# Optimization experiments

Measured on AMD Instinct MI355X. Metric: run time of the kernel, lower is better.

Reference implementation:

```python
import jax, jax.numpy as jnp
import numpy as np

P = 8    # patch_size
N = 16   # n_patches
WS = 32  # window_size


def setup_inputs() -> dict:
    key = jax.random.key(0)
    k1, k2 = jax.random.split(key)
    B, C, H, W = 8, 12, 512, 512
    return {
        "data_real": jax.random.normal(k1, (B, C, H, W), dtype=jnp.float32),
        "data_imag": jax.random.normal(k2, (B, C, H, W), dtype=jnp.float32),
        "ref_x": 248,
        "ref_y": 248,
    }


def reference(data_real, data_imag, ref_x, ref_y):
    p, n, ws = P, N, WS
    # complex64 represented as trailing real/imag axis (matches torch.view_as_real)
    data = jnp.stack([data_real, data_imag], axis=-1)  # [B,C,H,W,2]
    B, C, H, W, _ = data.shape

    # reference patch at (ref_x, ref_y)
    ref = data[:, :, ref_x:ref_x + p, ref_y:ref_y + p, :]  # [B,C,p,p,2]

    # clamped search window (static Python ints -> static shapes)
    wx0 = max(ref_x - ws // 2, 0); wx1 = min(ref_x + ws // 2, H)
    wy0 = max(ref_y - ws // 2, 0); wy1 = min(ref_y + ws // 2, W)
    win = data[:, :, wx0:wx1, wy0:wy1, :]  # [B,C,Wh,Ww,2]
    Wh, Ww = win.shape[2], win.shape[3]
    Ph, Pw = Wh - p + 1, Ww - p + 1

    # all sliding patches in the window, vectorized via fancy indexing
    ix = jnp.arange(Ph)[:, None] + jnp.arange(p)[None, :]  # [Ph,p]
    iy = jnp.arange(Pw)[:, None] + jnp.arange(p)[None, :]  # [Pw,p]
    patches = win[:, :, ix[:, None, :, None], iy[None, :, None, :], :]  # [B,C,Ph,Pw,p,p,2]

    # mse_loss over view_as_real == 0.5 * mean(|diff|^2) over p*p complex elems
    diff = patches - ref[:, :, None, None]
    dists = 0.5 * jnp.mean(diff * diff, axis=(-3, -2, -1))  # [B,C,Ph,Pw]

    M = Ph * Pw  # row-major (x outer, y inner) matches the torch loop order
    dists = dists.reshape(B, C, M)
    pats = patches.reshape(B, C, M, p * p, 2)

    slot = jnp.arange(n)

    def select(dv, pv):  # dv: [M], pv: [M, p*p, 2]
        def step(carry, inp):
            nd, ns = carry
            di, pi = inp
            mask = nd > di                      # candidate slots
            oh = (slot == jnp.argmax(mask)) & jnp.any(mask)  # first True slot
            nd = jnp.where(oh, di, nd)
            ns = jnp.where(oh[:, None, None], pi, ns)
            return (nd, ns), None

        init = (jnp.full((n,), 1e33, dtype=dv.dtype),
                jnp.zeros((n, p * p, 2), dtype=pv.dtype))
        (nd, ns), _ = jax.lax.scan(step, init, (dv, pv))
        return ns

    # independent sequential top-n insertion per (batch, contrast)
    sims = jax.vmap(jax.vmap(select))(dists, pats)  # [B,C,n,p*p,2]
    return sims
```

## Files before the change

### kernel.cpp

```cpp
#include <hip/hip_runtime.h>
#include <math.h>

#define PP    8
#define NSEL  16
#define WSZ   32

__global__ __launch_bounds__(256) void patches_select_kernel(
    const float* __restrict__ d_re,
    const float* __restrict__ d_im,
    const int*   __restrict__ p_rx,
    const int*   __restrict__ p_ry,
    float*       __restrict__ out,
    int H, int W)
{
    const int bc  = blockIdx.x;
    const int tid = threadIdx.x;

    const int rx = p_rx[0];
    const int ry = p_ry[0];
    const int wx0 = max(rx - WSZ / 2, 0);
    const int wx1 = min(rx + WSZ / 2, H);
    const int wy0 = max(ry - WSZ / 2, 0);
    const int wy1 = min(ry + WSZ / 2, W);
    const int Wh = wx1 - wx0;
    const int Ww = wy1 - wy0;
    const int Ph = Wh - PP + 1;
    const int Pw = Ww - PP + 1;
    const int M  = Ph * Pw;
    const int Mpad = (M + 15) & ~15;

    __shared__ float sre[WSZ][WSZ];
    __shared__ float sim[WSZ][WSZ];
    __shared__ float sref[PP][PP][2];
    __shared__ float dists[WSZ * WSZ];
    __shared__ int   selIdx[NSEL];

    const size_t plane = (size_t)H * W;
    const float* baseR = d_re + (size_t)bc * plane;
    const float* baseI = d_im + (size_t)bc * plane;

    for (int t = tid; t < Wh * Ww; t += 256) {
        const int i = t / Ww, j = t - i * Ww;
        const size_t g = (size_t)(wx0 + i) * W + (wy0 + j);
        sre[i][j] = baseR[g];
        sim[i][j] = baseI[g];
    }
    for (int t = tid; t < PP * PP; t += 256) {
        const int i = t / PP, j = t - i * PP;
        const size_t g = (size_t)(rx + i) * W + (ry + j);
        sref[i][j][0] = baseR[g];
        sref[i][j][1] = baseI[g];
    }
    if (tid < 16 && M + tid < Mpad) dists[M + tid] = INFINITY;
    __syncthreads();

    for (int m = tid; m < M; m += 256) {
        const int pi = m / Pw, pj = m - pi * Pw;
        float r[8];
#pragma unroll
        for (int j = 0; j < 8; ++j) r[j] = 0.0f;
#pragma unroll
        for (int k = 0; k < 16; ++k) {
            const int dx  = k >> 1;
            const int dyb = (k & 1) * 4;
#pragma unroll
            for (int j = 0; j < 8; ++j) {
                const int dy   = dyb + (j >> 1);
                const int comp = j & 1;
                const float w  = comp ? sim[pi + dx][pj + dy] : sre[pi + dx][pj + dy];
                const float rf = sref[dx][dy][comp];
                const float dl = __fsub_rn(w, rf);
                const float sq = __fmul_rn(dl, dl);
                r[j] = __fadd_rn(r[j], sq);
            }
        }
        const float s0 = __fadd_rn(__fadd_rn(r[0], r[1]), __fadd_rn(r[2], r[3]));
        const float s1 = __fadd_rn(__fadd_rn(r[4], r[5]), __fadd_rn(r[6], r[7]));
        const float S  = __fadd_rn(s0, s1);
        dists[m] = S * (1.0f / 256.0f);
    }
    __syncthreads();

    if (tid < 64) {
        float nd  = (tid < NSEL) ? 1e33f : -1.0f;
        int   mi  = -1;
        float cur[16];
#pragma unroll
        for (int u = 0; u < 16; ++u) cur[u] = dists[u];
        for (int m0 = 0; m0 < Mpad; m0 += 16) {
            float nxt[16];
            const int nb = m0 + 16;
            if (nb < Mpad) {
#pragma unroll
                for (int u = 0; u < 16; ++u) nxt[u] = dists[nb + u];
            } else {
#pragma unroll
                for (int u = 0; u < 16; ++u) nxt[u] = INFINITY;
            }
#pragma unroll
            for (int u = 0; u < 16; ++u) {
                const unsigned long long mask = __ballot(nd > cur[u]);
                const int first = __ffsll(mask) - 1;
                if (tid == first) { nd = cur[u]; mi = m0 + u; }
            }
#pragma unroll
            for (int u = 0; u < 16; ++u) cur[u] = nxt[u];
        }
        if (tid < NSEL) selIdx[tid] = mi;
    }
    __syncthreads();

    float* obase = out + (size_t)bc * (NSEL * PP * PP * 2);
    for (int t = tid; t < NSEL * PP * PP * 2; t += 256) {
        const int slot = t >> 7;
        const int rem  = t & 127;
        const int k    = rem >> 1;
        const int comp = rem & 1;
        const int m    = selIdx[slot];
        float v = 0.0f;
        if (m >= 0) {
            const int pi = m / Pw, pj = m - pi * Pw;
            const int dx = k >> 3, dy = k & 7;
            v = comp ? sim[pi + dx][pj + dy] : sre[pi + dx][pj + dy];
        }
        obase[t] = v;
    }
}

extern "C" void kernel_launch(void* const* d_in, const int* in_sizes, int n_in,
                              void* d_out, int out_size, void* d_ws, size_t ws_size,
                              hipStream_t stream) {
    const float* d_re = (const float*)d_in[0];
    const float* d_im = (const float*)d_in[1];
    const int*   p_rx = (const int*)d_in[2];
    const int*   p_ry = (const int*)d_in[3];
    float* out = (float*)d_out;

    const int H = 512, W = 512;
    const int BC = in_sizes[0] / (H * W);

    patches_select_kernel<<<BC, 256, 0, stream>>>(d_re, d_im, p_rx, p_ry, out, H, W);
}
```

Measured before the change: 197.1 us.

## Interleave window in shared memory, skip non-inserting blocks in top-n scan

```diff
diff --git a/kernel.cpp b/kernel.cpp
--- a/kernel.cpp
+++ b/kernel.cpp
@@ -4,6 +4,14 @@
 #define PP    8
 #define NSEL  16
 #define WSZ   32
+
+__device__ __forceinline__ float min16(const float* a) {
+    const float m0 = fminf(fminf(a[0],  a[1]),  fminf(a[2],  a[3]));
+    const float m1 = fminf(fminf(a[4],  a[5]),  fminf(a[6],  a[7]));
+    const float m2 = fminf(fminf(a[8],  a[9]),  fminf(a[10], a[11]));
+    const float m3 = fminf(fminf(a[12], a[13]), fminf(a[14], a[15]));
+    return fminf(fminf(m0, m1), fminf(m2, m3));
+}
 
 __global__ __launch_bounds__(256) void patches_select_kernel(
     const float* __restrict__ d_re,
@@ -29,24 +37,32 @@
     const int M  = Ph * Pw;
     const int Mpad = (M + 15) & ~15;
 
-    __shared__ float sre[WSZ][WSZ];
-    __shared__ float sim[WSZ][WSZ];
+    __shared__ float swin[WSZ][WSZ][2];
     __shared__ float sref[PP][PP][2];
     __shared__ float dists[WSZ * WSZ];
-    __shared__ int   selIdx[NSEL];
+    __shared__ int   selPK[NSEL];
 
     const size_t plane = (size_t)H * W;
     const float* baseR = d_re + (size_t)bc * plane;
     const float* baseI = d_im + (size_t)bc * plane;
 
-    for (int t = tid; t < Wh * Ww; t += 256) {
-        const int i = t / Ww, j = t - i * Ww;
-        const size_t g = (size_t)(wx0 + i) * W + (wy0 + j);
-        sre[i][j] = baseR[g];
-        sim[i][j] = baseI[g];
+    if (Ww == WSZ) {
+        for (int t = tid; t < Wh * WSZ; t += 256) {
+            const int i = t >> 5, j = t & 31;
+            const size_t g = (size_t)(wx0 + i) * W + (wy0 + j);
+            swin[i][j][0] = baseR[g];
+            swin[i][j][1] = baseI[g];
+        }
+    } else {
+        for (int t = tid; t < Wh * Ww; t += 256) {
+            const int i = t / Ww, j = t - i * Ww;
+            const size_t g = (size_t)(wx0 + i) * W + (wy0 + j);
+            swin[i][j][0] = baseR[g];
+            swin[i][j][1] = baseI[g];
+        }
     }
     for (int t = tid; t < PP * PP; t += 256) {
-        const int i = t / PP, j = t - i * PP;
+        const int i = t >> 3, j = t & 7;
         const size_t g = (size_t)(rx + i) * W + (ry + j);
         sref[i][j][0] = baseR[g];
         sref[i][j][1] = baseI[g];
@@ -64,14 +80,14 @@
             const int dx  = k >> 1;
             const int dyb = (k & 1) * 4;
 #pragma unroll
-            for (int j = 0; j < 8; ++j) {
-                const int dy   = dyb + (j >> 1);
-                const int comp = j & 1;
-                const float w  = comp ? sim[pi + dx][pj + dy] : sre[pi + dx][pj + dy];
-                const float rf = sref[dx][dy][comp];
-                const float dl = __fsub_rn(w, rf);
-                const float sq = __fmul_rn(dl, dl);
-                r[j] = __fadd_rn(r[j], sq);
+            for (int dd = 0; dd < 4; ++dd) {
+                const int dy = dyb + dd;
+                const float2 wv = *reinterpret_cast<const float2*>(&swin[pi + dx][pj + dy][0]);
+                const float2 rv = *reinterpret_cast<const float2*>(&sref[dx][dy][0]);
+                const float dre = __fsub_rn(wv.x, rv.x);
+                const float dim = __fsub_rn(wv.y, rv.y);
+                r[2 * dd + 0] = __fadd_rn(r[2 * dd + 0], __fmul_rn(dre, dre));
+                r[2 * dd + 1] = __fadd_rn(r[2 * dd + 1], __fmul_rn(dim, dim));
             }
         }
         const float s0 = __fadd_rn(__fadd_rn(r[0], r[1]), __fadd_rn(r[2], r[3]));
@@ -87,6 +103,7 @@
         float cur[16];
 #pragma unroll
         for (int u = 0; u < 16; ++u) cur[u] = dists[u];
+        float cb = min16(cur);
         for (int m0 = 0; m0 < Mpad; m0 += 16) {
             float nxt[16];
             const int nb = m0 + 16;
@@ -97,16 +114,24 @@
 #pragma unroll
                 for (int u = 0; u < 16; ++u) nxt[u] = INFINITY;
             }
+            const float nbmin = min16(nxt);
+            if (__ballot(nd > cb)) {
 #pragma unroll
-            for (int u = 0; u < 16; ++u) {
-                const unsigned long long mask = __ballot(nd > cur[u]);
-                const int first = __ffsll(mask) - 1;
-                if (tid == first) { nd = cur[u]; mi = m0 + u; }
+                for (int u = 0; u < 16; ++u) {
+                    const unsigned long long mask = __ballot(nd > cur[u]);
+                    const int first = __ffsll(mask) - 1;
+                    if (tid == first) { nd = cur[u]; mi = m0 + u; }
+                }
             }
 #pragma unroll
             for (int u = 0; u < 16; ++u) cur[u] = nxt[u];
+            cb = nbmin;
         }
-        if (tid < NSEL) selIdx[tid] = mi;
+        if (tid < NSEL) {
+            int pk = -1;
+            if (mi >= 0) { const int pi = mi / Pw; pk = (pi << 8) | (mi - pi * Pw); }
+            selPK[tid] = pk;
+        }
     }
     __syncthreads();
 
@@ -116,12 +141,12 @@
         const int rem  = t & 127;
         const int k    = rem >> 1;
         const int comp = rem & 1;
-        const int m    = selIdx[slot];
+        const int pk   = selPK[slot];
         float v = 0.0f;
-        if (m >= 0) {
-            const int pi = m / Pw, pj = m - pi * Pw;
+        if (pk >= 0) {
+            const int pi = pk >> 8, pj = pk & 255;
             const int dx = k >> 3, dy = k & 7;
-            v = comp ? sim[pi + dx][pj + dy] : sre[pi + dx][pj + dy];
+            v = swin[pi + dx][pj + dy][comp];
         }
         obase[t] = v;
     }
```

Measured after the change: 196.9 us. Within noise of the previous version (-0.1%).
